# Performance work log

Hardware: AMD Instinct MI355X
Metric: run time of the kernel (lower is better)

The kernel has to match this reference:

```python
import jax, jax.numpy as jnp
import numpy as np


def setup_inputs() -> dict:
    key = jax.random.key(0)
    k1, k2, k3, k4 = jax.random.split(key, 4)
    B, N, L, H, E = 2, 128, 128, 8, 64
    queries = jax.random.normal(k1, (B, N, L, H, E), dtype=jnp.float32)
    keys = jax.random.normal(k2, (B, N, L, H, E), dtype=jnp.float32)
    values = jax.random.normal(k3, (B, N, L, H, E), dtype=jnp.float32)
    # multiplicative spatial adjacency mask [B, N, M]
    attn_mask = jax.random.uniform(k4, (B, N, N), dtype=jnp.float32)
    return {"queries": queries, "keys": keys, "values": values, "attn_mask": attn_mask}


def reference(queries, keys, values, attn_mask):
    # queries/keys/values: [B, N, L, H, E]; attn_mask: [B, N, M]
    E = queries.shape[-1]
    scale = 1.0 / jnp.sqrt(jnp.asarray(E, queries.dtype))
    # --- temporal attention (per node, over time L) ---
    scores_t = jnp.einsum('bnlhe,bnshe->bnhls', queries, keys)  # [B,N,H,L,S]
    A_t = jax.nn.softmax(scale * scores_t, axis=-1)
    # dropout is identity at inference (Keras default training=False)
    V_t = jnp.einsum('bnhls,bnshd->bnlhd', A_t, values)  # [B,N,L,H,D]
    # --- spatial attention (per timestep, over nodes N) ---
    scores_s = jnp.einsum('bnlhe,bmlhe->blhnm', queries, keys)  # [B,L,H,N,M]
    scores_s = scores_s * attn_mask[:, None, None, :, :]        # multiplicative adjacency mask
    A_s = jax.nn.softmax(scale * scores_s, axis=-1)
    V = jnp.einsum('blhnm,bmlhd->bnlhd', A_s, V_t)  # [B,N,L,H,D]
    return V
```

## Files before the change

kernel.cpp:

```cpp
#include <hip/hip_runtime.h>

static constexpr int Bb = 2, Nn = 128, Ll = 128, Hh = 8, Ee = 64;
static constexpr float SCALE = 0.125f;

typedef short short8 __attribute__((ext_vector_type(8)));
typedef short short4v __attribute__((ext_vector_type(4)));
typedef float float4v __attribute__((ext_vector_type(4)));

#define MFMA16(a, b, c) __builtin_amdgcn_mfma_f32_16x16x32_bf16(a, b, c, 0, 0, 0)

__device__ inline float4 gload4(const float* p) {
  float4 r;
  asm volatile("global_load_dwordx4 %0, %1, off" : "=v"(r) : "v"(p) : "memory");
  return r;
}
__device__ inline float gload1(const float* p) {
  float r;
  asm volatile("global_load_dword %0, %1, off" : "=v"(r) : "v"(p) : "memory");
  return r;
}
#define WAIT_VM(N)                                    \
  do {                                                \
    asm volatile("s_waitcnt vmcnt(" #N ")" ::: "memory"); \
    __builtin_amdgcn_sched_barrier(0);                \
  } while (0)

__device__ inline unsigned short bf16_rne(float f) {
  unsigned u = __builtin_bit_cast(unsigned, f);
  u += 0x7FFFu + ((u >> 16) & 1u);
  return (unsigned short)(u >> 16);
}

__device__ inline void split4(float4 a, short4v& hi, short4v& lo) {
  float f[4] = {a.x, a.y, a.z, a.w};
#pragma unroll
  for (int j = 0; j < 4; ++j) {
    unsigned u = __builtin_bit_cast(unsigned, f[j]);
    unsigned short h = (unsigned short)(u >> 16);
    hi[j] = (short)h;
    float hf = __builtin_bit_cast(float, (unsigned)h << 16);
    lo[j] = (short)bf16_rne(f[j] - hf);
  }
}

__device__ inline void split8(float4 a, float4 b, short8& hi, short8& lo) {
  float f[8] = {a.x, a.y, a.z, a.w, b.x, b.y, b.z, b.w};
#pragma unroll
  for (int j = 0; j < 8; ++j) {
    unsigned u = __builtin_bit_cast(unsigned, f[j]);
    unsigned short h = (unsigned short)(u >> 16);
    hi[j] = (short)h;
    float hf = __builtin_bit_cast(float, (unsigned)h << 16);
    lo[j] = (short)bf16_rne(f[j] - hf);
  }
}

__device__ inline short8 pack4(const unsigned* p) {
  union { unsigned u[4]; short8 s; } t;
  t.u[0] = p[0]; t.u[1] = p[1]; t.u[2] = p[2]; t.u[3] = p[3];
  return t.s;
}

__device__ inline void lds_barrier() {
  __builtin_amdgcn_sched_barrier(0);
  asm volatile("s_waitcnt lgkmcnt(0)" ::: "memory");
  __builtin_amdgcn_s_barrier();
  __builtin_amdgcn_sched_barrier(0);
}

__device__ __forceinline__ void st_attn_body(
    const float* __restrict__ Qp, const float* __restrict__ Kp,
    const float* __restrict__ Vp, const float* __restrict__ Mp,
    float* __restrict__ Op, int idx_stride, int row_stride, bool HAS_MASK);

template <bool HAS_MASK>
__global__ __launch_bounds__(512, 3) void st_attn(
    const float* __restrict__ Qp, const float* __restrict__ Kp,
    const float* __restrict__ Vp, const float* __restrict__ Mp,
    float* __restrict__ Op, int idx_stride, int row_stride) {
  __shared__ __align__(16) unsigned short Pb[128 * 130];
  __shared__ __align__(16) unsigned short Vb[64 * 130];

  const int g = blockIdx.x;
  const int b = g >> 10;
  const int idx = (g >> 3) & 127;
  const int h = g & 7;
  const int base = b * (Nn * Ll * Hh * Ee) + idx * idx_stride + h * Ee;

  const int tid = threadIdx.x;
  const int wave = tid >> 6;
  const int lane = tid & 63;
  const int tx = lane & 15;
  const int quad = lane >> 4;
  const int rowbase = wave * 16;
  const int rowb = rowbase + quad * 4;

  const int mb = b * (Nn * Nn);

  float4 kL[4], qL[4], vL[4];
  float mv[8][4];
#pragma unroll
  for (int it = 0; it < 4; ++it) {
    const int i4 = tid + it * 512;
    kL[it] = gload4(Kp + base + (i4 >> 4) * row_stride + ((i4 & 15) << 2));
  }
  {
    const float* qr = Qp + base + (rowbase + tx) * row_stride;
#pragma unroll
    for (int ks = 0; ks < 2; ++ks) {
      qL[ks * 2 + 0] = gload4(qr + ks * 32 + quad * 8);
      qL[ks * 2 + 1] = gload4(qr + ks * 32 + quad * 8 + 4);
    }
  }
  if constexpr (HAS_MASK) {
#pragma unroll
    for (int ct = 0; ct < 8; ++ct)
#pragma unroll
      for (int e = 0; e < 4; ++e)
        mv[ct][e] = gload1(Mp + mb + (rowb + e) * 128 + ct * 16 + tx);
  }
#pragma unroll
  for (int it = 0; it < 4; ++it) {
    const int i4 = tid + it * 512;
    vL[it] = gload4(Vp + base + (i4 >> 4) * row_stride + ((i4 & 15) << 2));
  }

  if constexpr (HAS_MASK) WAIT_VM(36);
  else                    WAIT_VM(4);

#pragma unroll
  for (int it = 0; it < 4; ++it) {
    const int i4 = tid + it * 512;
    const int r = i4 >> 4;
    const int d0 = (i4 & 15) << 2;
    const int vs = d0 >> 3;
    const int idxk =
        ((((r >> 4) * 8 + vs) * 16 + (r & 15)) ^ vs) * 8 + (d0 & 7);
    short4v h4, l4;
    split4(kL[it], h4, l4);
    *(short4v*)(Pb + idxk) = h4;
    *(short4v*)(Pb + idxk + 8192) = l4;
  }

  short8 qhi[2], qlo[2];
#pragma unroll
  for (int ks = 0; ks < 2; ++ks)
    split8(qL[ks * 2 + 0], qL[ks * 2 + 1], qhi[ks], qlo[ks]);

  lds_barrier();

  float4v acc[8];
#pragma unroll
  for (int ct = 0; ct < 8; ++ct) acc[ct] = (float4v)(0.0f);

  const short8* KS8 = (const short8*)Pb;
#pragma unroll
  for (int ct = 0; ct < 8; ++ct) {
#pragma unroll
    for (int ks = 0; ks < 2; ++ks) {
      const int vs = ks * 4 + quad;
      const int fi = (((ct * 8 + vs) * 16 + tx) ^ vs);
      const short8 khi = KS8[fi];
      const short8 klo = KS8[fi + 1024];
      acc[ct] = MFMA16(qhi[ks], khi, acc[ct]);
      acc[ct] = MFMA16(qhi[ks], klo, acc[ct]);
      acc[ct] = MFMA16(qlo[ks], khi, acc[ct]);
    }
  }

  if constexpr (HAS_MASK) WAIT_VM(4);

  float rowsum[4] = {0.f, 0.f, 0.f, 0.f};
#pragma unroll
  for (int ct = 0; ct < 8; ++ct) {
#pragma unroll
    for (int e = 0; e < 4; ++e) {
      float p = acc[ct][e] * SCALE;
      if (HAS_MASK) p *= mv[ct][e];
      p = __expf(p);
      rowsum[e] += p;
      acc[ct][e] = p;
    }
  }

  float inv[4];
#pragma unroll
  for (int e = 0; e < 4; ++e) {
    float s = rowsum[e];
#pragma unroll
    for (int d = 1; d < 16; d <<= 1) s += __shfl_xor(s, d);
    inv[e] = 1.0f / s;
  }

  lds_barrier();

#pragma unroll
  for (int ct = 0; ct < 8; ++ct) {
    const int col = ct * 16 + tx;
#pragma unroll
    for (int e = 0; e < 4; ++e)
      Pb[(rowb + e) * 130 + col] = bf16_rne(acc[ct][e]);
  }

  WAIT_VM(0);
#pragma unroll
  for (int it = 0; it < 4; ++it) {
    const int i4 = tid + it * 512;
    const int c = i4 >> 4;
    const int d0 = (i4 & 15) << 2;
    const float4 v = vL[it];
    Vb[(d0 + 0) * 130 + c] = bf16_rne(v.x);
    Vb[(d0 + 1) * 130 + c] = bf16_rne(v.y);
    Vb[(d0 + 2) * 130 + c] = bf16_rne(v.z);
    Vb[(d0 + 3) * 130 + c] = bf16_rne(v.w);
  }

  __syncthreads();

  float4v accO[4];
#pragma unroll
  for (int dt = 0; dt < 4; ++dt) accO[dt] = (float4v)(0.0f);

#pragma unroll
  for (int ks = 0; ks < 4; ++ks) {
    const unsigned* pw =
        (const unsigned*)Pb + (rowbase + tx) * 65 + ks * 16 + quad * 4;
    const short8 pA = pack4(pw);
#pragma unroll
    for (int dt = 0; dt < 4; ++dt) {
      const unsigned* vw =
          (const unsigned*)Vb + (dt * 16 + tx) * 65 + ks * 16 + quad * 4;
      const short8 vB = pack4(vw);
      accO[dt] = MFMA16(pA, vB, accO[dt]);
    }
  }

#pragma unroll
  for (int dt = 0; dt < 4; ++dt) {
#pragma unroll
    for (int e = 0; e < 4; ++e) {
      Op[base + (rowb + e) * row_stride + dt * 16 + tx] =
          accO[dt][e] * inv[e];
    }
  }
}

extern "C" void kernel_launch(void* const* d_in, const int* in_sizes, int n_in,
                              void* d_out, int out_size, void* d_ws,
                              size_t ws_size, hipStream_t stream) {
  const float* Q = (const float*)d_in[0];
  const float* K = (const float*)d_in[1];
  const float* V = (const float*)d_in[2];
  const float* M = (const float*)d_in[3];
  float* out = (float*)d_out;
  float* Vt = (float*)d_ws;

  dim3 grid(Bb * Nn * Hh), blk(512);
  st_attn<false><<<grid, blk, 0, stream>>>(Q, K, V, nullptr, Vt,
                                           Ll * Hh * Ee ,
                                           Hh * Ee );
  st_attn<true><<<grid, blk, 0, stream>>>(Q, K, Vt, M, out,
                                          Hh * Ee ,
                                          Ll * Hh * Ee );
}
```

Measured before the change: 271.0 us.

## Store intermediate temporal output as bf16 in spatial-friendly layout

```diff
diff --git a/kernel.cpp b/kernel.cpp
--- a/kernel.cpp
+++ b/kernel.cpp
@@ -19,10 +19,10 @@
   asm volatile("global_load_dword %0, %1, off" : "=v"(r) : "v"(p) : "memory");
   return r;
 }
-#define WAIT_VM(N)                                    \
-  do {                                                \
+#define WAIT_VM(N)                                        \
+  do {                                                    \
     asm volatile("s_waitcnt vmcnt(" #N ")" ::: "memory"); \
-    __builtin_amdgcn_sched_barrier(0);                \
+    __builtin_amdgcn_sched_barrier(0);                    \
   } while (0)
 
 __device__ inline unsigned short bf16_rne(float f) {
@@ -68,16 +68,11 @@
   __builtin_amdgcn_sched_barrier(0);
 }
 
-__device__ __forceinline__ void st_attn_body(
-    const float* __restrict__ Qp, const float* __restrict__ Kp,
-    const float* __restrict__ Vp, const float* __restrict__ Mp,
-    float* __restrict__ Op, int idx_stride, int row_stride, bool HAS_MASK);
-
-template <bool HAS_MASK>
+template <bool SPATIAL>
 __global__ __launch_bounds__(512, 3) void st_attn(
     const float* __restrict__ Qp, const float* __restrict__ Kp,
-    const float* __restrict__ Vp, const float* __restrict__ Mp,
-    float* __restrict__ Op, int idx_stride, int row_stride) {
+    const void* __restrict__ Vp, const float* __restrict__ Mp,
+    void* __restrict__ Op, int idx_stride, int row_stride) {
   __shared__ __align__(16) unsigned short Pb[128 * 130];
   __shared__ __align__(16) unsigned short Vb[64 * 130];
 
@@ -94,7 +89,6 @@
   const int quad = lane >> 4;
   const int rowbase = wave * 16;
   const int rowb = rowbase + quad * 4;
-
   const int mb = b * (Nn * Nn);
 
   float4 kL[4], qL[4], vL[4];
@@ -112,21 +106,31 @@
       qL[ks * 2 + 1] = gload4(qr + ks * 32 + quad * 8 + 4);
     }
   }
-  if constexpr (HAS_MASK) {
+  if constexpr (SPATIAL) {
+    const unsigned short* Vt = (const unsigned short*)Vp;
+    const unsigned short* vsl =
+        Vt + ((b * Ll + idx) * Hh + h) * (Nn * Ee);
+#pragma unroll
+    for (int it = 0; it < 2; ++it) {
+      const int i8 = tid + it * 512;
+      vL[it] = gload4((const float*)(vsl + i8 * 8));
+    }
 #pragma unroll
     for (int ct = 0; ct < 8; ++ct)
 #pragma unroll
       for (int e = 0; e < 4; ++e)
         mv[ct][e] = gload1(Mp + mb + (rowb + e) * 128 + ct * 16 + tx);
-  }
-#pragma unroll
-  for (int it = 0; it < 4; ++it) {
-    const int i4 = tid + it * 512;
-    vL[it] = gload4(Vp + base + (i4 >> 4) * row_stride + ((i4 & 15) << 2));
-  }
-
-  if constexpr (HAS_MASK) WAIT_VM(36);
-  else                    WAIT_VM(4);
+  } else {
+    const float* Vf = (const float*)Vp;
+#pragma unroll
+    for (int it = 0; it < 4; ++it) {
+      const int i4 = tid + it * 512;
+      vL[it] = gload4(Vf + base + (i4 >> 4) * row_stride + ((i4 & 15) << 2));
+    }
+  }
+
+  if constexpr (SPATIAL) WAIT_VM(34);
+  else                   WAIT_VM(4);
 
 #pragma unroll
   for (int it = 0; it < 4; ++it) {
@@ -168,7 +172,7 @@
     }
   }
 
-  if constexpr (HAS_MASK) WAIT_VM(4);
+  if constexpr (SPATIAL) WAIT_VM(0);
 
   float rowsum[4] = {0.f, 0.f, 0.f, 0.f};
 #pragma unroll
@@ -176,7 +180,7 @@
 #pragma unroll
     for (int e = 0; e < 4; ++e) {
       float p = acc[ct][e] * SCALE;
-      if (HAS_MASK) p *= mv[ct][e];
+      if (SPATIAL) p *= mv[ct][e];
       p = __expf(p);
       rowsum[e] += p;
       acc[ct][e] = p;
@@ -202,17 +206,30 @@
       Pb[(rowb + e) * 130 + col] = bf16_rne(acc[ct][e]);
   }
 
-  WAIT_VM(0);
-#pragma unroll
-  for (int it = 0; it < 4; ++it) {
-    const int i4 = tid + it * 512;
-    const int c = i4 >> 4;
-    const int d0 = (i4 & 15) << 2;
-    const float4 v = vL[it];
-    Vb[(d0 + 0) * 130 + c] = bf16_rne(v.x);
-    Vb[(d0 + 1) * 130 + c] = bf16_rne(v.y);
-    Vb[(d0 + 2) * 130 + c] = bf16_rne(v.z);
-    Vb[(d0 + 3) * 130 + c] = bf16_rne(v.w);
+  if constexpr (SPATIAL) {
+#pragma unroll
+    for (int it = 0; it < 2; ++it) {
+      const int i8 = tid + it * 512;
+      const int m = i8 >> 3;
+      const int e0 = (i8 & 7) * 8;
+      union { float4 f; unsigned short u[8]; } t;
+      t.f = vL[it];
+#pragma unroll
+      for (int j = 0; j < 8; ++j) Vb[(e0 + j) * 130 + m] = t.u[j];
+    }
+  } else {
+    WAIT_VM(0);
+#pragma unroll
+    for (int it = 0; it < 4; ++it) {
+      const int i4 = tid + it * 512;
+      const int c = i4 >> 4;
+      const int d0 = (i4 & 15) << 2;
+      const float4 v = vL[it];
+      Vb[(d0 + 0) * 130 + c] = bf16_rne(v.x);
+      Vb[(d0 + 1) * 130 + c] = bf16_rne(v.y);
+      Vb[(d0 + 2) * 130 + c] = bf16_rne(v.z);
+      Vb[(d0 + 3) * 130 + c] = bf16_rne(v.w);
+    }
   }
 
   __syncthreads();
@@ -235,13 +252,22 @@
     }
   }
 
-#pragma unroll
-  for (int dt = 0; dt < 4; ++dt) {
-#pragma unroll
-    for (int e = 0; e < 4; ++e) {
-      Op[base + (rowb + e) * row_stride + dt * 16 + tx] =
-          accO[dt][e] * inv[e];
-    }
+  if constexpr (SPATIAL) {
+    float* O = (float*)Op;
+#pragma unroll
+    for (int dt = 0; dt < 4; ++dt)
+#pragma unroll
+      for (int e = 0; e < 4; ++e)
+        O[base + (rowb + e) * row_stride + dt * 16 + tx] =
+            accO[dt][e] * inv[e];
+  } else {
+    unsigned short* O = (unsigned short*)Op;
+#pragma unroll
+    for (int dt = 0; dt < 4; ++dt)
+#pragma unroll
+      for (int e = 0; e < 4; ++e)
+        O[((b * Ll + (rowb + e)) * Hh + h) * (Nn * Ee) + idx * Ee + dt * 16 +
+          tx] = bf16_rne(accO[dt][e] * inv[e]);
   }
 }
 
@@ -253,13 +279,13 @@
   const float* V = (const float*)d_in[2];
   const float* M = (const float*)d_in[3];
   float* out = (float*)d_out;
-  float* Vt = (float*)d_ws;
+  unsigned short* Vt = (unsigned short*)d_ws;
 
   dim3 grid(Bb * Nn * Hh), blk(512);
-  st_attn<false><<<grid, blk, 0, stream>>>(Q, K, V, nullptr, Vt,
-                                           Ll * Hh * Ee ,
+  st_attn<false><<<grid, blk, 0, stream>>>(Q, K, (const void*)V, nullptr,
+                                           (void*)Vt, Ll * Hh * Ee ,
                                            Hh * Ee );
-  st_attn<true><<<grid, blk, 0, stream>>>(Q, K, Vt, M, out,
-                                          Hh * Ee ,
+  st_attn<true><<<grid, blk, 0, stream>>>(Q, K, (const void*)Vt, M,
+                                          (void*)out, Hh * Ee ,
                                           Ll * Hh * Ee );
 }
```

Result: faster. 264.7 us (-2.3%).
